# Performance work log

Measured on AMD Instinct MI355X. Metric: run time of the kernel, lower is better.

Reference implementation:

```python
import jax, jax.numpy as jnp
import numpy as np

N, L, D = 8, 256, 256  # batch, length, hidden
DP = D + 1             # flag=True appends bias column


def setup_inputs() -> dict:
    key = jax.random.key(0)
    ks = jax.random.split(key, 7)
    s = 0.02  # xavier-like init scale
    return {
        "layer1": jax.random.normal(ks[0], (N, L, D), jnp.float32),
        "layer2": jax.random.normal(ks[1], (N, L, D), jnp.float32),
        "h1": jax.random.normal(ks[2], (N, L, D), jnp.float32),
        "h2": jax.random.normal(ks[3], (N, L, D), jnp.float32),
        "W_1": jax.random.normal(ks[4], (DP, DP, D), jnp.float32) * s,
        "W_2": jax.random.normal(ks[5], (DP, DP, D), jnp.float32) * s,
        "W_3": jax.random.normal(ks[6], (D, D), jnp.float32) * s,
    }


def reference(layer1, layer2, h1, h2, W_1, W_2, W_3):
    n, l, _ = layer1.shape
    ones = jnp.ones((n, l, 1), layer1.dtype)
    l1 = jnp.concatenate([layer1, ones], axis=-1)  # [n, L, D+1]
    l2 = jnp.concatenate([layer2, ones], axis=-1)  # [n, L, D+1]
    # factorized triaffine: two nijc intermediates, then rank contraction
    layer_l = jnp.einsum('nia,abc,njb,nic->nijc', l1, W_1, l2, h1, optimize='optimal')
    layer_r = jnp.einsum('nia,abc,njb,nic->nijc', l1, W_2, l2, h2, optimize='optimal')
    return jnp.einsum('nijc,cd,nijd->nij', layer_l, W_3, layer_r, optimize='optimal')
```

## Files before the change

kernel.cpp:

```cpp
#include <hip/hip_runtime.h>

typedef __attribute__((ext_vector_type(4))) float f32x4;
typedef __attribute__((ext_vector_type(8))) short s16x8;

#define MTOTW 65792

__device__ __forceinline__ short f2bf(float f) {
    unsigned u = __builtin_bit_cast(unsigned, f);
    u = (u + 0x7fffu + ((u >> 16) & 1u)) >> 16;
    return (short)u;
}

__device__ __forceinline__ void gl16(const void* g, void* l) {
    __builtin_amdgcn_global_load_lds(
        (const __attribute__((address_space(1))) unsigned int*)g,
        (__attribute__((address_space(3))) unsigned int*)l, 16, 0, 0);
}

__global__ __launch_bounds__(256) void conv_bf16(
    const float* __restrict__ a, const float* __restrict__ b,
    short* __restrict__ ao, short* __restrict__ bo)
{
    int i = blockIdx.x * 256 + threadIdx.x;
    const int HALF = 131072;
    float4 v; short* dst;
    if (i < HALF) { v = ((const float4*)a)[i]; dst = ao + (size_t)i * 4; }
    else          { v = ((const float4*)b)[i - HALF]; dst = bo + (size_t)(i - HALF) * 4; }
    short4 o; o.x = f2bf(v.x); o.y = f2bf(v.y); o.z = f2bf(v.z); o.w = f2bf(v.w);
    *(short4*)dst = o;
}

__global__ __launch_bounds__(256) void prep_w3t(
    const float* __restrict__ W3, short* __restrict__ W3t)
{
    __shared__ float ld[32][33];
    int t = threadIdx.x, bx = blockIdx.x;
    int c0 = (bx >> 3) * 32, d0 = (bx & 7) * 32;
    int cr = t >> 3, dq = t & 7;
    float4 v = *(const float4*)&W3[(size_t)(c0 + cr) * 256 + d0 + dq * 4];
    ld[cr][dq*4+0] = v.x; ld[cr][dq*4+1] = v.y; ld[cr][dq*4+2] = v.z; ld[cr][dq*4+3] = v.w;
    __syncthreads();
    int dr = t >> 3, cq = t & 7;
    short4 o;
    o.x = f2bf(ld[cq*4+0][dr]); o.y = f2bf(ld[cq*4+1][dr]);
    o.z = f2bf(ld[cq*4+2][dr]); o.w = f2bf(ld[cq*4+3][dr]);
    *(short4*)&W3t[(size_t)(d0 + dr) * 256 + c0 + cq * 4] = o;
}

__global__ __launch_bounds__(256) void prep_wtail(
    const float* __restrict__ W1, const float* __restrict__ W2,
    short* __restrict__ Wtp1, short* __restrict__ Wtp2)
{
    __shared__ float ld[32][33];
    int t = threadIdx.x, bx = blockIdx.x;
    const float* W = blockIdx.y ? W2 : W1;
    short* Wtp = blockIdx.y ? Wtp2 : Wtp1;
    int a0 = (bx >> 3) * 32, c0 = (bx & 7) * 32;
    int ar = t >> 3, cq = t & 7;
    float4 v = *(const float4*)&W[(size_t)(a0 + ar) * MTOTW + 65536 + c0 + cq * 4];
    ld[ar][cq*4+0] = v.x; ld[ar][cq*4+1] = v.y; ld[ar][cq*4+2] = v.z; ld[ar][cq*4+3] = v.w;
    __syncthreads();
    int cr = t >> 3, aq = t & 7;
    short4 o;
    o.x = f2bf(ld[aq*4+0][cr]); o.y = f2bf(ld[aq*4+1][cr]);
    o.z = f2bf(ld[aq*4+2][cr]); o.w = f2bf(ld[aq*4+3][cr]);
    *(short4*)&Wtp[(size_t)(c0 + cr) * 256 + a0 + aq * 4] = o;
}

__global__ __launch_bounds__(256) void prep_wp(
    const float* __restrict__ W1, const float* __restrict__ W2,
    short* __restrict__ Wp1, short* __restrict__ Wp2)
{
    __shared__ float ld[32][33];
    int t = threadIdx.x, bx = blockIdx.x;
    int b = blockIdx.y;
    const float* W = blockIdx.z ? W2 : W1;
    short* Wp = blockIdx.z ? Wp2 : Wp1;
    int a0 = (bx >> 3) * 32, c0 = (bx & 7) * 32;
    int ar = t >> 3, cq = t & 7;
    float4 v = *(const float4*)&W[(size_t)(a0 + ar) * MTOTW + (size_t)b * 256 + c0 + cq * 4];
    ld[ar][cq*4+0] = v.x; ld[ar][cq*4+1] = v.y; ld[ar][cq*4+2] = v.z; ld[ar][cq*4+3] = v.w;
    __syncthreads();
    int cr = t >> 3, aq = t & 7;
    short4 o;
    o.x = f2bf(ld[aq*4+0][cr]); o.y = f2bf(ld[aq*4+1][cr]);
    o.z = f2bf(ld[aq*4+2][cr]); o.w = f2bf(ld[aq*4+3][cr]);
    *(short4*)&Wp[((size_t)(c0 + cr) * 256 + b) * 256 + a0 + aq * 4] = o;
}

__global__ __launch_bounds__(256, 2) void tail_mfma(
    const short* __restrict__ l1b,
    const short* __restrict__ Wtp1, const short* __restrict__ Wtp2,
    const float* __restrict__ W1, const float* __restrict__ W2,
    float* __restrict__ tail1, float* __restrict__ tail2)
{
    __shared__ __align__(16) short Al[128 * 32];
    __shared__ __align__(16) short Bl[128 * 32];
    int t = threadIdx.x, w = t >> 6, lane = t & 63;
    int l4 = lane >> 2, kq = lane & 3;
    int rt = blockIdx.x, nt = blockIdx.y, ten = blockIdx.z;
    const short* Wtp = ten ? Wtp2 : Wtp1;
    const float* Wf = ten ? W2 : W1;
    float* tail = ten ? tail2 : tail1;
    const short* Ab = l1b + (size_t)(rt * 128) * 256;
    const short* Bb = Wtp + (size_t)(nt * 128) * 256;

    f32x4 acc[4][4] = {};
    int m0w = (w >> 1) * 64, n0w = (w & 1) * 64;

    for (int k0 = 0; k0 < 256; k0 += 32) {
        __syncthreads();
        #pragma unroll
        for (int q = 0; q < 4; ++q) {
            int seg = w * 4 + q;
            if (seg < 8)
                gl16(Ab + (size_t)(seg * 16 + l4) * 256 + k0 + kq * 8, &Al[seg * 512]);
            else
                gl16(Bb + (size_t)((seg - 8) * 16 + l4) * 256 + k0 + kq * 8, &Bl[(seg - 8) * 512]);
        }
        __syncthreads();
        s16x8 af[4], bf[4];
        #pragma unroll
        for (int i = 0; i < 4; ++i) {
            af[i] = *(const s16x8*)&Al[(m0w + i * 16 + (lane & 15)) * 32 + (lane >> 4) * 8];
            bf[i] = *(const s16x8*)&Bl[(n0w + i * 16 + (lane & 15)) * 32 + (lane >> 4) * 8];
        }
        #pragma unroll
        for (int mi = 0; mi < 4; ++mi)
            #pragma unroll
            for (int ni = 0; ni < 4; ++ni)
                acc[mi][ni] = __builtin_amdgcn_mfma_f32_16x16x32_bf16(af[mi], bf[ni], acc[mi][ni], 0, 0, 0);
    }
    #pragma unroll
    for (int ni = 0; ni < 4; ++ni) {
        int c = nt * 128 + n0w + ni * 16 + (lane & 15);
        float tl = Wf[(size_t)256 * MTOTW + 65536 + c];
        #pragma unroll
        for (int mi = 0; mi < 4; ++mi) {
            int r = rt * 128 + m0w + mi * 16 + (lane >> 4) * 4;
            #pragma unroll
            for (int reg = 0; reg < 4; ++reg)
                tail[(size_t)(r + reg) * 256 + c] = acc[mi][ni][reg] + tl;
        }
    }
}

__global__ __launch_bounds__(256, 3) void stage1(
    const short* __restrict__ l1b,
    const short* __restrict__ Wp1, const short* __restrict__ Wp2,
    const float* __restrict__ W1, const float* __restrict__ W2,
    short* __restrict__ T1, short* __restrict__ T2, int row0)
{
    __shared__ __align__(16) short S[16384];
    int t = threadIdx.x, w = t >> 6, lane = t & 63;
    int l4 = lane >> 2, kq = lane & 3;

    unsigned gdx = gridDim.x;
    unsigned orig = blockIdx.x + gdx * (blockIdx.y + 2u * blockIdx.z);
    unsigned nwg = gdx * 1024u;
    unsigned swz = (orig & 7u) * (nwg >> 3) + (orig >> 3);
    int rt = swz & (gdx - 1u);
    unsigned rest = swz / gdx;
    int bt = rest & 1, zc = rest >> 1;

    int c = zc >> 1, ten = zc & 1;
    const short* Wp = ten ? Wp2 : Wp1;
    const float* Wf = ten ? W2 : W1;
    short* T = ten ? T2 : T1;
    int r0g = row0 + rt * 128;
    int b0 = bt * 128;
    const short* Ab = l1b + (size_t)r0g * 256;
    const short* Bb = Wp + ((size_t)c * 256 + b0) * 256;

    f32x4 acc[4][4] = {};
    int m0w = (w >> 1) * 64, n0w = (w & 1) * 64;

    for (int k0 = 0; k0 < 256; k0 += 32) {
        __syncthreads();
        #pragma unroll
        for (int q = 0; q < 4; ++q) {
            int seg = w * 4 + q;
            if (seg < 8)
                gl16(Ab + (size_t)(seg * 16 + l4) * 256 + k0 + kq * 8, &S[seg * 512]);
            else
                gl16(Bb + (size_t)((seg - 8) * 16 + l4) * 256 + k0 + kq * 8, &S[4096 + (seg - 8) * 512]);
        }
        __syncthreads();
        s16x8 af[4], bf[4];
        #pragma unroll
        for (int i = 0; i < 4; ++i) {
            af[i] = *(const s16x8*)&S[(m0w + i * 16 + (lane & 15)) * 32 + (lane >> 4) * 8];
            bf[i] = *(const s16x8*)&S[4096 + (n0w + i * 16 + (lane & 15)) * 32 + (lane >> 4) * 8];
        }
        #pragma unroll
        for (int mi = 0; mi < 4; ++mi)
            #pragma unroll
            for (int ni = 0; ni < 4; ++ni)
                acc[mi][ni] = __builtin_amdgcn_mfma_f32_16x16x32_bf16(af[mi], bf[ni], acc[mi][ni], 0, 0, 0);
    }
    __syncthreads();

    short* Cw = &S[w * 4096];
    #pragma unroll
    for (int ni = 0; ni < 4; ++ni) {
        int b = b0 + n0w + ni * 16 + (lane & 15);
        float tl = Wf[(size_t)256 * MTOTW + (size_t)b * 256 + c];
        #pragma unroll
        for (int mi = 0; mi < 4; ++mi)
            #pragma unroll
            for (int reg = 0; reg < 4; ++reg) {
                int lr = mi * 16 + (lane >> 4) * 4 + reg;
                int lc = ni * 16 + (lane & 15);
                Cw[lr * 64 + lc] = f2bf(acc[mi][ni][reg] + tl);
            }
    }
    #pragma unroll
    for (int s = 0; s < 8; ++s) {
        int row = s * 8 + (lane >> 3);
        int co = (lane & 7) * 8;
        int rl = rt * 128 + m0w + row;
        int gb = b0 + n0w + co;
        *(int4*)&T[((size_t)rl * 256 + c) * 256 + gb] = *(int4*)&Cw[row * 64 + co];
    }
}

__global__ __launch_bounds__(256, 2) void stage2(
    const short* __restrict__ l2b,
    const short* __restrict__ T1, const short* __restrict__ T2,
    const float* __restrict__ tail1, const float* __restrict__ tail2,
    const float* __restrict__ h1, const float* __restrict__ h2,
    const short* __restrict__ W3t, float* __restrict__ out, int row0)
{
    __shared__ __align__(16) short S2[26624];
    int t = threadIdx.x, w = t >> 6, lane = t & 63;
    int l4 = lane >> 2, kq = lane & 3;

    unsigned orig = blockIdx.x + (blockIdx.y << 2);
    unsigned nwg = gridDim.y << 2;
    unsigned swz = (orig & 7u) * (nwg >> 3) + (orig >> 3);
    int jt = swz & 3, rl = swz >> 2;

    int rg = row0 + rl, n = rg >> 8, j0 = jt * 64;
    const short* Arow = l2b + ((size_t)n * 256 + j0) * 256;
    const short* Tt1 = T1 + (size_t)rl * 65536;
    const short* Tt2 = T2 + (size_t)rl * 65536;
    int n0w = w * 64;

    f32x4 acc1[4][4] = {}, acc2[4][4] = {};
    for (int k0 = 0; k0 < 256; k0 += 32) {
        __syncthreads();
        #pragma unroll
        for (int q = 0; q < 9; ++q) {
            int seg = w * 9 + q;
            const short* gb; short* lb;
            if (seg < 4)       { gb = Arow + (size_t)(seg * 16 + l4) * 256;        lb = &S2[seg * 512]; }
            else if (seg < 20) { int s = seg - 4;  gb = Tt1 + (size_t)(s * 16 + l4) * 256; lb = &S2[2048 + s * 512]; }
            else               { int s = seg - 20; gb = Tt2 + (size_t)(s * 16 + l4) * 256; lb = &S2[10240 + s * 512]; }
            gl16(gb + k0 + kq * 8, lb);
        }
        __syncthreads();
        s16x8 af[4], b1[4], b2[4];
        #pragma unroll
        for (int i = 0; i < 4; ++i) {
            af[i] = *(const s16x8*)&S2[(i * 16 + (lane & 15)) * 32 + (lane >> 4) * 8];
            b1[i] = *(const s16x8*)&S2[2048 + (n0w + i * 16 + (lane & 15)) * 32 + (lane >> 4) * 8];
            b2[i] = *(const s16x8*)&S2[10240 + (n0w + i * 16 + (lane & 15)) * 32 + (lane >> 4) * 8];
        }
        #pragma unroll
        for (int mi = 0; mi < 4; ++mi)
            #pragma unroll
            for (int ni = 0; ni < 4; ++ni) {
                acc1[mi][ni] = __builtin_amdgcn_mfma_f32_16x16x32_bf16(af[mi], b1[ni], acc1[mi][ni], 0, 0, 0);
                acc2[mi][ni] = __builtin_amdgcn_mfma_f32_16x16x32_bf16(af[mi], b2[ni], acc2[mi][ni], 0, 0, 0);
            }
    }
    __syncthreads();

    short* V1 = S2;
    f32x4 v2[4][4];
    #pragma unroll
    for (int ni = 0; ni < 4; ++ni) {
        int c = n0w + ni * 16 + (lane & 15);
        float hh1 = h1[(size_t)rg * 256 + c], tl1 = tail1[(size_t)rg * 256 + c];
        float hh2 = h2[(size_t)rg * 256 + c], tl2 = tail2[(size_t)rg * 256 + c];
        #pragma unroll
        for (int mi = 0; mi < 4; ++mi)
            #pragma unroll
            for (int reg = 0; reg < 4; ++reg) {
                int j = mi * 16 + (lane >> 4) * 4 + reg;
                V1[j * 264 + c] = f2bf(hh1 * (acc1[mi][ni][reg] + tl1));
                v2[mi][ni][reg] = hh2 * (acc2[mi][ni][reg] + tl2);
            }
    }
    __syncthreads();

    f32x4 accP[4][4] = {};
    for (int k0 = 0; k0 < 256; k0 += 32) {
        __syncthreads();
        #pragma unroll
        for (int q = 0; q < 4; ++q) {
            int s = w * 4 + q;
            gl16(W3t + (size_t)(s * 16 + l4) * 256 + k0 + kq * 8, &S2[18432 + s * 512]);
        }
        __syncthreads();
        s16x8 af[4], bf[4];
        #pragma unroll
        for (int i = 0; i < 4; ++i) {
            af[i] = *(const s16x8*)&V1[(i * 16 + (lane & 15)) * 264 + k0 + (lane >> 4) * 8];
            bf[i] = *(const s16x8*)&S2[18432 + (n0w + i * 16 + (lane & 15)) * 32 + (lane >> 4) * 8];
        }
        #pragma unroll
        for (int mi = 0; mi < 4; ++mi)
            #pragma unroll
            for (int ni = 0; ni < 4; ++ni)
                accP[mi][ni] = __builtin_amdgcn_mfma_f32_16x16x32_bf16(af[mi], bf[ni], accP[mi][ni], 0, 0, 0);
    }

    float* part = (float*)&S2[16896];
    #pragma unroll
    for (int mi = 0; mi < 4; ++mi)
        #pragma unroll
        for (int reg = 0; reg < 4; ++reg) {
            float s = 0.f;
            #pragma unroll
            for (int ni = 0; ni < 4; ++ni) s += accP[mi][ni][reg] * v2[mi][ni][reg];
            s += __shfl_xor(s, 1); s += __shfl_xor(s, 2);
            s += __shfl_xor(s, 4); s += __shfl_xor(s, 8);
            if ((lane & 15) == 0)
                part[(mi * 16 + (lane >> 4) * 4 + reg) * 4 + w] = s;
        }
    __syncthreads();
    if (t < 64)
        out[(size_t)rg * 256 + j0 + t] = part[t*4] + part[t*4+1] + part[t*4+2] + part[t*4+3];
}

extern "C" void kernel_launch(void* const* d_in, const int* in_sizes, int n_in,
                              void* d_out, int out_size, void* d_ws, size_t ws_size,
                              hipStream_t stream) {
    const float* layer1 = (const float*)d_in[0];
    const float* layer2 = (const float*)d_in[1];
    const float* h1     = (const float*)d_in[2];
    const float* h2     = (const float*)d_in[3];
    const float* W1     = (const float*)d_in[4];
    const float* W2     = (const float*)d_in[5];
    const float* W3     = (const float*)d_in[6];
    float* out = (float*)d_out;

    short* Wp1  = (short*)d_ws;
    short* Wp2  = Wp1 + 16777216;
    short* l1b  = Wp2 + 16777216;
    short* l2b  = l1b + 524288;
    short* W3t  = l2b + 524288;
    short* Wtp1 = W3t + 65536;
    short* Wtp2 = Wtp1 + 65536;
    float* tail1 = (float*)(Wtp2 + 65536);
    float* tail2 = tail1 + 524288;
    short* T1   = (short*)(tail2 + 524288);
    const size_t head = (size_t)(16777216*2 + 524288*2 + 65536*3) * 2 + (size_t)524288 * 2 * 4;
    int chunk = 2048;
    while (head + (size_t)chunk * 262144 > ws_size && chunk > 128) chunk >>= 1;
    short* T2 = T1 + (size_t)chunk * 65536;

    conv_bf16<<<1024, 256, 0, stream>>>(layer1, layer2, l1b, l2b);
    prep_w3t<<<64, 256, 0, stream>>>(W3, W3t);
    prep_wtail<<<dim3(64, 2), 256, 0, stream>>>(W1, W2, Wtp1, Wtp2);
    prep_wp<<<dim3(64, 256, 2), 256, 0, stream>>>(W1, W2, Wp1, Wp2);
    tail_mfma<<<dim3(16, 2, 2), 256, 0, stream>>>(l1b, Wtp1, Wtp2, W1, W2, tail1, tail2);

    for (int row0 = 0; row0 < 2048; row0 += chunk) {
        stage1<<<dim3(chunk / 128, 2, 512), 256, 0, stream>>>(
            l1b, Wp1, Wp2, W1, W2, T1, T2, row0);
        stage2<<<dim3(4, chunk), 256, 0, stream>>>(
            l2b, T1, T2, tail1, tail2, h1, h2, W3t, out, row0);
    }
}
```

Measured before the change: 767.2 us.

## Double K-tile depth to 64 and XOR-swizzle LDS tiles in stage1/stage2

Changes the K step of all three GEMM loops from 32 to 64, which halves the number of barrier pairs and load rounds. Each 64-wide row of the LDS tile is XOR-swizzled on its 16-byte chunks so the MFMA fragment reads avoid bank conflicts. Stage2's shared memory grows from about 53KB to 74KB, which may reduce occupancy below the two blocks per CU that its launch bounds request. The W3 tile buffer moves to a new offset that must not overlap V1 or the partial-sum region.

```diff
diff --git a/kernel.cpp b/kernel.cpp
--- a/kernel.cpp
+++ b/kernel.cpp
@@ -16,6 +16,7 @@
         (const __attribute__((address_space(1))) unsigned int*)g,
         (__attribute__((address_space(3))) unsigned int*)l, 16, 0, 0);
 }
+
 
 __global__ __launch_bounds__(256) void conv_bf16(
     const float* __restrict__ a, const float* __restrict__ b,
@@ -153,7 +154,9 @@
 {
     __shared__ __align__(16) short S[16384];
     int t = threadIdx.x, w = t >> 6, lane = t & 63;
-    int l4 = lane >> 2, kq = lane & 3;
+    int srow8 = lane >> 3;
+    int sch   = (lane & 7) ^ srow8;
+    int fr    = lane & 15, fb7 = lane & 7;
 
     unsigned gdx = gridDim.x;
     unsigned orig = blockIdx.x + gdx * (blockIdx.y + 2u * blockIdx.z);
@@ -175,28 +178,32 @@
     f32x4 acc[4][4] = {};
     int m0w = (w >> 1) * 64, n0w = (w & 1) * 64;
 
-    for (int k0 = 0; k0 < 256; k0 += 32) {
-        __syncthreads();
-        #pragma unroll
-        for (int q = 0; q < 4; ++q) {
-            int seg = w * 4 + q;
-            if (seg < 8)
-                gl16(Ab + (size_t)(seg * 16 + l4) * 256 + k0 + kq * 8, &S[seg * 512]);
-            else
-                gl16(Bb + (size_t)((seg - 8) * 16 + l4) * 256 + k0 + kq * 8, &S[4096 + (seg - 8) * 512]);
-        }
-        __syncthreads();
-        s16x8 af[4], bf[4];
-        #pragma unroll
-        for (int i = 0; i < 4; ++i) {
-            af[i] = *(const s16x8*)&S[(m0w + i * 16 + (lane & 15)) * 32 + (lane >> 4) * 8];
-            bf[i] = *(const s16x8*)&S[4096 + (n0w + i * 16 + (lane & 15)) * 32 + (lane >> 4) * 8];
-        }
-        #pragma unroll
-        for (int mi = 0; mi < 4; ++mi)
-            #pragma unroll
-            for (int ni = 0; ni < 4; ++ni)
-                acc[mi][ni] = __builtin_amdgcn_mfma_f32_16x16x32_bf16(af[mi], bf[ni], acc[mi][ni], 0, 0, 0);
+    for (int kt = 0; kt < 4; ++kt) {
+        int k0 = kt * 64;
+        __syncthreads();
+        #pragma unroll
+        for (int q = 0; q < 8; ++q) {
+            int seg = w * 8 + q;
+            int rloc = (seg & 15) * 8 + srow8;
+            const short* gb = (seg < 16) ? Ab : Bb;
+            gl16(gb + (size_t)rloc * 256 + k0 + sch * 8, &S[seg * 512]);
+        }
+        __syncthreads();
+        #pragma unroll
+        for (int ss = 0; ss < 2; ++ss) {
+            int cx = ((ss * 4 + (lane >> 4)) ^ fb7) * 8;
+            s16x8 af[4], bf[4];
+            #pragma unroll
+            for (int i = 0; i < 4; ++i) {
+                af[i] = *(const s16x8*)&S[(m0w + i * 16 + fr) * 64 + cx];
+                bf[i] = *(const s16x8*)&S[8192 + (n0w + i * 16 + fr) * 64 + cx];
+            }
+            #pragma unroll
+            for (int mi = 0; mi < 4; ++mi)
+                #pragma unroll
+                for (int ni = 0; ni < 4; ++ni)
+                    acc[mi][ni] = __builtin_amdgcn_mfma_f32_16x16x32_bf16(af[mi], bf[ni], acc[mi][ni], 0, 0, 0);
+        }
     }
     __syncthreads();
 
@@ -231,9 +238,11 @@
     const float* __restrict__ h1, const float* __restrict__ h2,
     const short* __restrict__ W3t, float* __restrict__ out, int row0)
 {
-    __shared__ __align__(16) short S2[26624];
+    __shared__ __align__(16) short S2[36864];
     int t = threadIdx.x, w = t >> 6, lane = t & 63;
-    int l4 = lane >> 2, kq = lane & 3;
+    int srow8 = lane >> 3;
+    int sch   = (lane & 7) ^ srow8;
+    int fr    = lane & 15, fb7 = lane & 7;
 
     unsigned orig = blockIdx.x + (blockIdx.y << 2);
     unsigned nwg = gridDim.y << 2;
@@ -247,32 +256,37 @@
     int n0w = w * 64;
 
     f32x4 acc1[4][4] = {}, acc2[4][4] = {};
-    for (int k0 = 0; k0 < 256; k0 += 32) {
-        __syncthreads();
-        #pragma unroll
-        for (int q = 0; q < 9; ++q) {
-            int seg = w * 9 + q;
-            const short* gb; short* lb;
-            if (seg < 4)       { gb = Arow + (size_t)(seg * 16 + l4) * 256;        lb = &S2[seg * 512]; }
-            else if (seg < 20) { int s = seg - 4;  gb = Tt1 + (size_t)(s * 16 + l4) * 256; lb = &S2[2048 + s * 512]; }
-            else               { int s = seg - 20; gb = Tt2 + (size_t)(s * 16 + l4) * 256; lb = &S2[10240 + s * 512]; }
-            gl16(gb + k0 + kq * 8, lb);
-        }
-        __syncthreads();
-        s16x8 af[4], b1[4], b2[4];
-        #pragma unroll
-        for (int i = 0; i < 4; ++i) {
-            af[i] = *(const s16x8*)&S2[(i * 16 + (lane & 15)) * 32 + (lane >> 4) * 8];
-            b1[i] = *(const s16x8*)&S2[2048 + (n0w + i * 16 + (lane & 15)) * 32 + (lane >> 4) * 8];
-            b2[i] = *(const s16x8*)&S2[10240 + (n0w + i * 16 + (lane & 15)) * 32 + (lane >> 4) * 8];
-        }
-        #pragma unroll
-        for (int mi = 0; mi < 4; ++mi)
-            #pragma unroll
-            for (int ni = 0; ni < 4; ++ni) {
-                acc1[mi][ni] = __builtin_amdgcn_mfma_f32_16x16x32_bf16(af[mi], b1[ni], acc1[mi][ni], 0, 0, 0);
-                acc2[mi][ni] = __builtin_amdgcn_mfma_f32_16x16x32_bf16(af[mi], b2[ni], acc2[mi][ni], 0, 0, 0);
-            }
+    for (int kt = 0; kt < 4; ++kt) {
+        int k0 = kt * 64;
+        __syncthreads();
+        #pragma unroll
+        for (int q = 0; q < 18; ++q) {
+            int seg = w * 18 + q;
+            const short* gb; short* lb; int rloc;
+            if (seg < 8)       { rloc = seg * 8 + srow8;        gb = Arow; lb = &S2[seg * 512]; }
+            else if (seg < 40) { rloc = (seg - 8) * 8 + srow8;  gb = Tt1;  lb = &S2[4096 + (seg - 8) * 512]; }
+            else               { rloc = (seg - 40) * 8 + srow8; gb = Tt2;  lb = &S2[20480 + (seg - 40) * 512]; }
+            gl16(gb + (size_t)rloc * 256 + k0 + sch * 8, lb);
+        }
+        __syncthreads();
+        #pragma unroll
+        for (int ss = 0; ss < 2; ++ss) {
+            int cx = ((ss * 4 + (lane >> 4)) ^ fb7) * 8;
+            s16x8 af[4], b1[4], b2[4];
+            #pragma unroll
+            for (int i = 0; i < 4; ++i) {
+                af[i] = *(const s16x8*)&S2[(i * 16 + fr) * 64 + cx];
+                b1[i] = *(const s16x8*)&S2[4096 + (n0w + i * 16 + fr) * 64 + cx];
+                b2[i] = *(const s16x8*)&S2[20480 + (n0w + i * 16 + fr) * 64 + cx];
+            }
+            #pragma unroll
+            for (int mi = 0; mi < 4; ++mi)
+                #pragma unroll
+                for (int ni = 0; ni < 4; ++ni) {
+                    acc1[mi][ni] = __builtin_amdgcn_mfma_f32_16x16x32_bf16(af[mi], b1[ni], acc1[mi][ni], 0, 0, 0);
+                    acc2[mi][ni] = __builtin_amdgcn_mfma_f32_16x16x32_bf16(af[mi], b2[ni], acc2[mi][ni], 0, 0, 0);
+                }
+        }
     }
     __syncthreads();
 
@@ -295,25 +309,31 @@
     __syncthreads();
 
     f32x4 accP[4][4] = {};
-    for (int k0 = 0; k0 < 256; k0 += 32) {
-        __syncthreads();
-        #pragma unroll
-        for (int q = 0; q < 4; ++q) {
-            int s = w * 4 + q;
-            gl16(W3t + (size_t)(s * 16 + l4) * 256 + k0 + kq * 8, &S2[18432 + s * 512]);
-        }
-        __syncthreads();
-        s16x8 af[4], bf[4];
-        #pragma unroll
-        for (int i = 0; i < 4; ++i) {
-            af[i] = *(const s16x8*)&V1[(i * 16 + (lane & 15)) * 264 + k0 + (lane >> 4) * 8];
-            bf[i] = *(const s16x8*)&S2[18432 + (n0w + i * 16 + (lane & 15)) * 32 + (lane >> 4) * 8];
-        }
-        #pragma unroll
-        for (int mi = 0; mi < 4; ++mi)
-            #pragma unroll
-            for (int ni = 0; ni < 4; ++ni)
-                accP[mi][ni] = __builtin_amdgcn_mfma_f32_16x16x32_bf16(af[mi], bf[ni], accP[mi][ni], 0, 0, 0);
+    for (int kt = 0; kt < 4; ++kt) {
+        int k0 = kt * 64;
+        __syncthreads();
+        #pragma unroll
+        for (int q = 0; q < 8; ++q) {
+            int seg = w * 8 + q;
+            int rloc = seg * 8 + srow8;
+            gl16(W3t + (size_t)rloc * 256 + k0 + sch * 8, &S2[20480 + seg * 512]);
+        }
+        __syncthreads();
+        #pragma unroll
+        for (int ss = 0; ss < 2; ++ss) {
+            int cx = ((ss * 4 + (lane >> 4)) ^ fb7) * 8;
+            s16x8 af[4], bf[4];
+            #pragma unroll
+            for (int i = 0; i < 4; ++i) {
+                af[i] = *(const s16x8*)&V1[(i * 16 + fr) * 264 + k0 + ss * 32 + (lane >> 4) * 8];
+                bf[i] = *(const s16x8*)&S2[20480 + (n0w + i * 16 + fr) * 64 + cx];
+            }
+            #pragma unroll
+            for (int mi = 0; mi < 4; ++mi)
+                #pragma unroll
+                for (int ni = 0; ni < 4; ++ni)
+                    accP[mi][ni] = __builtin_amdgcn_mfma_f32_16x16x32_bf16(af[mi], bf[ni], accP[mi][ni], 0, 0, 0);
+        }
     }
 
     float* part = (float*)&S2[16896];
```

Result: faster. 725.3 us (-5.5%).
